# Kernel tuning notes

Hardware: AMD Instinct MI355X
Metric: run time of the kernel (lower is better)

Reference implementation:

```python
import jax, jax.numpy as jnp
import numpy as np

NEG_SLOPE = 0.2  # PyG GATConv default leaky_relu slope
EPS = 1e-16


def gat_conv(x, W, att_src, att_dst, bias, src, dst, heads, out_ch, concat):
    """PyG-style GATConv (eval mode, self-loops already added).
    x: [N, F_in], W: [F_in, heads*out_ch], att_src/att_dst: [heads, out_ch], bias matches output.
    src/dst: [E] int edge endpoints (messages flow src -> dst).
    """
    N = x.shape[0]
    h = (x @ W).reshape(N, heads, out_ch)                 # [N, H, C]
    a_src = jnp.einsum('nhc,hc->nh', h, att_src)           # [N, H]
    a_dst = jnp.einsum('nhc,hc->nh', h, att_dst)           # [N, H]
    e = jax.nn.leaky_relu(a_src[src] + a_dst[dst], NEG_SLOPE)  # [E, H]
    # scatter-softmax over edges grouped by destination node
    emax = jax.ops.segment_max(e, dst, num_segments=N)     # [N, H]
    e = jnp.exp(e - emax[dst])
    denom = jax.ops.segment_sum(e, dst, num_segments=N)    # [N, H]
    alpha = e / (denom[dst] + EPS)                         # [E, H]
    msg = alpha[:, :, None] * h[src]                       # [E, H, C]
    out = jax.ops.segment_sum(msg, dst, num_segments=N)    # [N, H, C]
    out = out.reshape(N, heads * out_ch) if concat else out.mean(axis=1)
    return out + bias


def _add_self_loops(edge_index, N):
    loop = jnp.arange(N, dtype=edge_index.dtype)
    src = jnp.concatenate([edge_index[0], loop])
    dst = jnp.concatenate([edge_index[1], loop])
    return src, dst


def setup_inputs() -> dict:
    key = jax.random.key(0)
    ks = jax.random.split(key, 12)
    N, F_in, E = 100000, 256, 3200000
    H1, C1 = 2, 16
    C2 = 40  # num_classes
    x = jax.random.normal(ks[0], (N, F_in), dtype=jnp.float32)
    edge_index = jax.random.randint(ks[1], (2, E), 0, N, dtype=jnp.int32)
    s1 = 1.0 / np.sqrt(F_in)
    s2 = 1.0 / np.sqrt(H1 * C1)
    W1 = jax.random.normal(ks[2], (F_in, H1 * C1), dtype=jnp.float32) * s1
    att_src1 = jax.random.normal(ks[3], (H1, C1), dtype=jnp.float32) * s2
    att_dst1 = jax.random.normal(ks[4], (H1, C1), dtype=jnp.float32) * s2
    b1 = jnp.zeros((H1 * C1,), dtype=jnp.float32)
    W2 = jax.random.normal(ks[5], (H1 * C1, C2), dtype=jnp.float32) * s2
    att_src2 = jax.random.normal(ks[6], (1, C2), dtype=jnp.float32) * 0.15
    att_dst2 = jax.random.normal(ks[7], (1, C2), dtype=jnp.float32) * 0.15
    b2 = jnp.zeros((C2,), dtype=jnp.float32)
    return {"x": x, "edge_index": edge_index, "W1": W1, "att_src1": att_src1,
            "att_dst1": att_dst1, "b1": b1, "W2": W2, "att_src2": att_src2,
            "att_dst2": att_dst2, "b2": b2}


def reference(x, edge_index, W1, att_src1, att_dst1, b1, W2, att_src2, att_dst2, b2):
    N = x.shape[0]
    src, dst = _add_self_loops(edge_index, N)
    h = gat_conv(x, W1, att_src1, att_dst1, b1, src, dst, heads=2, out_ch=16, concat=True)
    h = jax.nn.relu(h)
    # F.dropout / attention dropout are identity in eval mode
    out = gat_conv(h, W2, att_src2, att_dst2, b2, src, dst, heads=1, out_ch=40, concat=False)
    return jax.nn.log_softmax(out, axis=1)
```

## Files before the change

### kernel.cpp

```cpp
#include <hip/hip_runtime.h>
#include <math.h>

#define FIN 256
#define F1  32
#define H1  2
#define C1  16
#define C2  40
#define MAXDEG 96
#define NEG_SLOPE 0.2f
#define GAT_EPS 1e-16f
#define G1_NODES 32
#define FILL_BLOCKS 2048

__device__ __forceinline__ float lrelu(float v) { return v >= 0.f ? v : NEG_SLOPE * v; }

__global__ __launch_bounds__(256) void k_fill_adj(const int* __restrict__ ei, int E, int N,
                                                  int* __restrict__ deg, int* __restrict__ adj) {
    int res = blockIdx.x & 7;
    int nper = (N + 7) >> 3;
    int lo = res * nper;
    int hi = min(N, lo + nper);
    int total = E + N;
    int stride = (gridDim.x >> 3) * blockDim.x;
    for (int j = (blockIdx.x >> 3) * blockDim.x + threadIdx.x; j < total; j += stride) {
        int d, s;
        if (j < E) {
            d = __builtin_nontemporal_load(&ei[E + j]);
            s = 0;
            if (d >= lo && d < hi) s = __builtin_nontemporal_load(&ei[j]);
        } else {
            d = j - E; s = d;
        }
        if (d >= lo && d < hi) {
            int pos = atomicAdd(&deg[d], 1);
            if (pos < MAXDEG) adj[d * MAXDEG + pos] = s;
        }
    }
}

__global__ __launch_bounds__(256) void k_gemm1(const float* __restrict__ x,
                                               const float* __restrict__ W1,
                                               const float* __restrict__ attS,
                                               const float* __restrict__ attD,
                                               float* __restrict__ h1,
                                               float* __restrict__ aS,
                                               float* __restrict__ aD, int N) {
    __shared__ float xs[G1_NODES * FIN];
    __shared__ float Ws[FIN * F1];
    int tid = threadIdx.x;
    int node0 = blockIdx.x * G1_NODES;

    const float4* W4 = (const float4*)W1;
    float4* Ws4 = (float4*)Ws;
    for (int i = tid; i < FIN * F1 / 4; i += 256) Ws4[i] = W4[i];

    const float4* x4 = (const float4*)x;
    float4* xs4 = (float4*)xs;
    for (int i = tid; i < G1_NODES * FIN / 4; i += 256) {
        int r = i >> 6;
        int n = node0 + r;
        float4 v = make_float4(0.f, 0.f, 0.f, 0.f);
        if (n < N) v = x4[(size_t)n * 64 + (i & 63)];
        xs4[i] = v;
    }
    __syncthreads();

    int ln = tid >> 3;
    int c0 = (tid & 7) * 4;
    float a0 = 0.f, a1 = 0.f, a2 = 0.f, a3 = 0.f;
    for (int k = 0; k < FIN; k += 4) {
        float4 xv = *(const float4*)&xs[ln * FIN + k];
        float4 w0 = *(const float4*)&Ws[(k + 0) * F1 + c0];
        float4 w1 = *(const float4*)&Ws[(k + 1) * F1 + c0];
        float4 w2 = *(const float4*)&Ws[(k + 2) * F1 + c0];
        float4 w3 = *(const float4*)&Ws[(k + 3) * F1 + c0];
        a0 += xv.x * w0.x + xv.y * w1.x + xv.z * w2.x + xv.w * w3.x;
        a1 += xv.x * w0.y + xv.y * w1.y + xv.z * w2.y + xv.w * w3.y;
        a2 += xv.x * w0.z + xv.y * w1.z + xv.z * w2.z + xv.w * w3.z;
        a3 += xv.x * w0.w + xv.y * w1.w + xv.z * w2.w + xv.w * w3.w;
    }

    float4 sv = *(const float4*)&attS[c0];
    float4 dv = *(const float4*)&attD[c0];
    float ps = a0 * sv.x + a1 * sv.y + a2 * sv.z + a3 * sv.w;
    float pd = a0 * dv.x + a1 * dv.y + a2 * dv.z + a3 * dv.w;
    ps += __shfl_xor(ps, 1); ps += __shfl_xor(ps, 2);
    pd += __shfl_xor(pd, 1); pd += __shfl_xor(pd, 2);
    float po = __shfl_xor(ps, 4);
    float qo = __shfl_xor(pd, 4);

    int n = node0 + ln;
    if (n < N) {
        *(float4*)&h1[(size_t)n * F1 + c0] = make_float4(a0, a1, a2, a3);
        if ((tid & 7) == 0) {
            *(float2*)&aS[2 * (size_t)n] = make_float2(ps, po);
            *(float2*)&aD[2 * (size_t)n] = make_float2(pd, qo);
        }
    }
}

__global__ __launch_bounds__(256) void k_agg1(const float* __restrict__ h1,
                                              const int* __restrict__ adj,
                                              const int* __restrict__ deg,
                                              const float* __restrict__ aS,
                                              const float* __restrict__ aD,
                                              const float* __restrict__ b1,
                                              float* __restrict__ h1r, int N) {
    int warp = threadIdx.x >> 6;
    int lane = threadIdx.x & 63;
    int node = blockIdx.x * 4 + warp;
    if (node >= N) return;
    int dg = min(deg[node], MAXDEG);
    float2 adp = *(const float2*)&aD[node * 2];
    const int* ap = adj + (size_t)node * MAXDEG;

    int s0 = 0, s1 = 0;
    float e00 = -INFINITY, e01 = -INFINITY, e10 = -INFINITY, e11 = -INFINITY;
    if (lane < dg) {
        s0 = ap[lane];
        float2 as = *(const float2*)&aS[2 * s0];
        e00 = lrelu(as.x + adp.x); e01 = lrelu(as.y + adp.y);
    }
    if (lane + 64 < dg) {
        s1 = ap[lane + 64];
        float2 as = *(const float2*)&aS[2 * s1];
        e10 = lrelu(as.x + adp.x); e11 = lrelu(as.y + adp.y);
    }
    float m0 = fmaxf(e00, e10), m1 = fmaxf(e01, e11);
#pragma unroll
    for (int off = 32; off; off >>= 1) {
        m0 = fmaxf(m0, __shfl_xor(m0, off));
        m1 = fmaxf(m1, __shfl_xor(m1, off));
    }
    float w00 = (lane < dg)      ? __expf(e00 - m0) : 0.f;
    float w01 = (lane < dg)      ? __expf(e01 - m1) : 0.f;
    float w10 = (lane + 64 < dg) ? __expf(e10 - m0) : 0.f;
    float w11 = (lane + 64 < dg) ? __expf(e11 - m1) : 0.f;
    float sw0 = w00 + w10, sw1 = w01 + w11;
#pragma unroll
    for (int off = 32; off; off >>= 1) {
        sw0 += __shfl_xor(sw0, off);
        sw1 += __shfl_xor(sw1, off);
    }

    int eg = lane >> 3;
    int cg = lane & 7;
    int head = cg >> 2;
    float4 acc = make_float4(0.f, 0.f, 0.f, 0.f);
    for (int j0 = 0; j0 < dg; j0 += 8) {
        int j = j0 + eg;
        int sl = j & 63;
        int s; float w;
        if (j0 < 64) {
            s = __shfl(s0, sl);
            float wA = __shfl(w00, sl);
            float wB = __shfl(w01, sl);
            w = head ? wB : wA;
        } else {
            s = __shfl(s1, sl);
            float wA = __shfl(w10, sl);
            float wB = __shfl(w11, sl);
            w = head ? wB : wA;
        }
        float4 hv = *(const float4*)&h1[(size_t)s * F1 + cg * 4];
        acc.x += w * hv.x; acc.y += w * hv.y; acc.z += w * hv.z; acc.w += w * hv.w;
    }
#pragma unroll
    for (int off = 8; off < 64; off <<= 1) {
        acc.x += __shfl_xor(acc.x, off);
        acc.y += __shfl_xor(acc.y, off);
        acc.z += __shfl_xor(acc.z, off);
        acc.w += __shfl_xor(acc.w, off);
    }
    if (eg == 0) {
        float swh = head ? sw1 : sw0;
        float inv = 1.f / (swh + GAT_EPS);
        float4 bv = *(const float4*)&b1[cg * 4];
        float4 o;
        o.x = fmaxf(acc.x * inv + bv.x, 0.f);
        o.y = fmaxf(acc.y * inv + bv.y, 0.f);
        o.z = fmaxf(acc.z * inv + bv.z, 0.f);
        o.w = fmaxf(acc.w * inv + bv.w, 0.f);
        *(float4*)&h1r[(size_t)node * F1 + cg * 4] = o;
    }
}

__global__ __launch_bounds__(320) void k_gemm2(const float* __restrict__ h1r,
                                               const float* __restrict__ W2,
                                               float* __restrict__ h2, int N) {
    __shared__ float hs[8 * F1];
    __shared__ float Ws[F1 * C2];
    int tid = threadIdx.x;
    int node0 = blockIdx.x * 8;
    for (int i = tid; i < F1 * C2; i += 320) Ws[i] = W2[i];
    if (tid < 8 * F1) {
        int r = tid >> 5;
        int n = node0 + r;
        hs[tid] = (n < N) ? h1r[(size_t)n * F1 + (tid & 31)] : 0.f;
    }
    __syncthreads();
    int node = tid / C2;
    int col  = tid - node * C2;
    int n = node0 + node;
    if (n < N) {
        float acc = 0.f;
#pragma unroll
        for (int k = 0; k < F1; k++) acc += hs[node * F1 + k] * Ws[k * C2 + col];
        h2[(size_t)n * C2 + col] = acc;
    }
}

__global__ void k_attdots2(const float* __restrict__ h2,
                           const float* __restrict__ attS, const float* __restrict__ attD,
                           float* __restrict__ aS, float* __restrict__ aD, int N) {
    int n = blockIdx.x * blockDim.x + threadIdx.x;
    if (n >= N) return;
    const float* hp = h2 + (size_t)n * C2;
    float s = 0.f, d = 0.f;
#pragma unroll
    for (int c = 0; c < C2; c++) { float v = hp[c]; s += v * attS[c]; d += v * attD[c]; }
    aS[n] = s; aD[n] = d;
}

__global__ __launch_bounds__(256) void k_agg2(const float* __restrict__ h2,
                                              const int* __restrict__ adj,
                                              const int* __restrict__ deg,
                                              const float* __restrict__ aS,
                                              const float* __restrict__ aD,
                                              const float* __restrict__ b2,
                                              float* __restrict__ out, int N) {
    int warp = threadIdx.x >> 6;
    int lane = threadIdx.x & 63;
    int node = blockIdx.x * 4 + warp;
    if (node >= N) return;
    int dg = min(deg[node], MAXDEG);
    float ad = aD[node];
    const int* ap = adj + (size_t)node * MAXDEG;

    int s0 = 0, s1 = 0;
    float e0 = -INFINITY, e1 = -INFINITY;
    if (lane < dg)      { s0 = ap[lane];      e0 = lrelu(aS[s0] + ad); }
    if (lane + 64 < dg) { s1 = ap[lane + 64]; e1 = lrelu(aS[s1] + ad); }
    float m = fmaxf(e0, e1);
#pragma unroll
    for (int off = 32; off; off >>= 1) m = fmaxf(m, __shfl_xor(m, off));
    float w0 = (lane < dg)      ? __expf(e0 - m) : 0.f;
    float w1 = (lane + 64 < dg) ? __expf(e1 - m) : 0.f;
    float sw = w0 + w1;
#pragma unroll
    for (int off = 32; off; off >>= 1) sw += __shfl_xor(sw, off);

    int eg = lane >> 3;
    int cg = lane & 7;
    float4 acc = make_float4(0.f, 0.f, 0.f, 0.f);
    float acc4 = 0.f;
    for (int j0 = 0; j0 < dg; j0 += 8) {
        int j = j0 + eg;
        int sl = j & 63;
        int s; float w;
        if (j0 < 64) { s = __shfl(s0, sl); w = __shfl(w0, sl); }
        else         { s = __shfl(s1, sl); w = __shfl(w1, sl); }
        const float* hp = &h2[(size_t)s * C2];
        float4 hv = *(const float4*)&hp[cg * 4];
        float  h5 = hp[32 + cg];
        acc.x += w * hv.x; acc.y += w * hv.y; acc.z += w * hv.z; acc.w += w * hv.w;
        acc4  += w * h5;
    }
#pragma unroll
    for (int off = 8; off < 64; off <<= 1) {
        acc.x += __shfl_xor(acc.x, off);
        acc.y += __shfl_xor(acc.y, off);
        acc.z += __shfl_xor(acc.z, off);
        acc.w += __shfl_xor(acc.w, off);
        acc4  += __shfl_xor(acc4, off);
    }
    float inv = 1.f / (sw + GAT_EPS);
    float4 bv = *(const float4*)&b2[cg * 4];
    float  b5 = b2[32 + cg];
    float v0 = acc.x * inv + bv.x;
    float v1 = acc.y * inv + bv.y;
    float v2 = acc.z * inv + bv.z;
    float v3 = acc.w * inv + bv.w;
    float v4 = acc4  * inv + b5;

    float lm = fmaxf(fmaxf(fmaxf(v0, v1), fmaxf(v2, v3)), v4);
#pragma unroll
    for (int off = 1; off < 8; off <<= 1) lm = fmaxf(lm, __shfl_xor(lm, off));
    float ex = __expf(v0 - lm) + __expf(v1 - lm) + __expf(v2 - lm) +
               __expf(v3 - lm) + __expf(v4 - lm);
#pragma unroll
    for (int off = 1; off < 8; off <<= 1) ex += __shfl_xor(ex, off);
    float lse = lm + __logf(ex);
    if (eg == 0) {
        float* op = out + (size_t)node * C2;
        float4 o = make_float4(v0 - lse, v1 - lse, v2 - lse, v3 - lse);
        *(float4*)&op[cg * 4] = o;
        op[32 + cg] = v4 - lse;
    }
}

extern "C" void kernel_launch(void* const* d_in, const int* in_sizes, int n_in,
                              void* d_out, int out_size, void* d_ws, size_t ws_size,
                              hipStream_t stream) {
    const float* x    = (const float*)d_in[0];
    const int*   ei   = (const int*)d_in[1];
    const float* W1   = (const float*)d_in[2];
    const float* aS1w = (const float*)d_in[3];
    const float* aD1w = (const float*)d_in[4];
    const float* b1   = (const float*)d_in[5];
    const float* W2   = (const float*)d_in[6];
    const float* aS2w = (const float*)d_in[7];
    const float* aD2w = (const float*)d_in[8];
    const float* b2   = (const float*)d_in[9];
    const int N = in_sizes[0] / FIN;
    const int E = in_sizes[1] / 2;

    char* ws = (char*)d_ws;
    size_t off = 0;
    auto alloc = [&](size_t bytes) -> void* {
        void* p = ws + off;
        off = (off + bytes + 511) & ~(size_t)511;
        return p;
    };
    int*   deg = (int*)alloc(sizeof(int) * (size_t)N);
    int*   adj = (int*)alloc(sizeof(int) * (size_t)N * MAXDEG);
    float* h1  = (float*)alloc(sizeof(float) * (size_t)N * F1);
    float* aS1 = (float*)alloc(sizeof(float) * (size_t)N * H1);
    float* aD1 = (float*)alloc(sizeof(float) * (size_t)N * H1);
    float* h1r = (float*)alloc(sizeof(float) * (size_t)N * F1);
    float* h2  = (float*)alloc(sizeof(float) * (size_t)N * C2);
    float* aS2 = (float*)alloc(sizeof(float) * (size_t)N);
    float* aD2 = (float*)alloc(sizeof(float) * (size_t)N);

    hipMemsetAsync(deg, 0, sizeof(int) * (size_t)N, stream);
    k_fill_adj<<<FILL_BLOCKS, 256, 0, stream>>>(ei, E, N, deg, adj);
    k_gemm1<<<(N + G1_NODES - 1) / G1_NODES, 256, 0, stream>>>(x, W1, aS1w, aD1w, h1, aS1, aD1, N);
    k_agg1<<<(N + 3) / 4, 256, 0, stream>>>(h1, adj, deg, aS1, aD1, b1, h1r, N);
    k_gemm2<<<(N + 7) / 8, 320, 0, stream>>>(h1r, W2, h2, N);
    k_attdots2<<<(N + 255) / 256, 256, 0, stream>>>(h2, aS2w, aD2w, aS2, aD2, N);
    k_agg2<<<(N + 3) / 4, 256, 0, stream>>>(h2, adj, deg, aS2, aD2, b2, (float*)d_out, N);
}
```

Measured before the change: 574.5 us.

## Merge adjacency fill with gemm1 and fuse layer-2 attention dots into gemm2

The adjacency-fill and first GEMM now run in one launch, with block ranges split between the two roles so the memory-bound atomic scatter can overlap the x@W1 compute. The gemm1 path drops its LDS staging and reads x and W1 straight from global memory through the cache. The separate attdots2 kernel is removed; gemm2 instead reduces the per-node att_src/att_dst dot products with LDS atomics and writes them directly, saving a pass over h2. The risks are that gemm1 without shared memory may become bound on global loads, and that the LDS float atomics add contention.

```diff
diff --git a/kernel.cpp b/kernel.cpp
--- a/kernel.cpp
+++ b/kernel.cpp
@@ -14,66 +14,56 @@
 
 __device__ __forceinline__ float lrelu(float v) { return v >= 0.f ? v : NEG_SLOPE * v; }
 
-__global__ __launch_bounds__(256) void k_fill_adj(const int* __restrict__ ei, int E, int N,
-                                                  int* __restrict__ deg, int* __restrict__ adj) {
-    int res = blockIdx.x & 7;
-    int nper = (N + 7) >> 3;
-    int lo = res * nper;
-    int hi = min(N, lo + nper);
-    int total = E + N;
-    int stride = (gridDim.x >> 3) * blockDim.x;
-    for (int j = (blockIdx.x >> 3) * blockDim.x + threadIdx.x; j < total; j += stride) {
-        int d, s;
-        if (j < E) {
-            d = __builtin_nontemporal_load(&ei[E + j]);
-            s = 0;
-            if (d >= lo && d < hi) s = __builtin_nontemporal_load(&ei[j]);
-        } else {
-            d = j - E; s = d;
-        }
-        if (d >= lo && d < hi) {
+__global__ __launch_bounds__(256) void k_fill_gemm1(const int* __restrict__ ei, int E,
+                                                    const float* __restrict__ x,
+                                                    const float* __restrict__ W1,
+                                                    const float* __restrict__ attS,
+                                                    const float* __restrict__ attD,
+                                                    int* __restrict__ deg,
+                                                    int* __restrict__ adj,
+                                                    float* __restrict__ h1,
+                                                    float* __restrict__ aS,
+                                                    float* __restrict__ aD, int N) {
+    if (blockIdx.x < FILL_BLOCKS) {
+        int res = blockIdx.x & 7;
+        int nper = (N + 7) >> 3;
+        int lo = res * nper;
+        int hi = min(N, lo + nper);
+        int total = E + N;
+        int stride = (FILL_BLOCKS >> 3) * 256;
+        for (int j = (blockIdx.x >> 3) * 256 + threadIdx.x; j < total; j += stride) {
+            int d, s;
+            if (j < E) {
+                d = __builtin_nontemporal_load(&ei[E + j]);
+                if (d < lo || d >= hi) continue;
+                s = __builtin_nontemporal_load(&ei[j]);
+            } else {
+                d = j - E; s = d;
+                if (d < lo || d >= hi) continue;
+            }
             int pos = atomicAdd(&deg[d], 1);
             if (pos < MAXDEG) adj[d * MAXDEG + pos] = s;
         }
-    }
-}
-
-__global__ __launch_bounds__(256) void k_gemm1(const float* __restrict__ x,
-                                               const float* __restrict__ W1,
-                                               const float* __restrict__ attS,
-                                               const float* __restrict__ attD,
-                                               float* __restrict__ h1,
-                                               float* __restrict__ aS,
-                                               float* __restrict__ aD, int N) {
-    __shared__ float xs[G1_NODES * FIN];
-    __shared__ float Ws[FIN * F1];
+        return;
+    }
+
     int tid = threadIdx.x;
-    int node0 = blockIdx.x * G1_NODES;
-
-    const float4* W4 = (const float4*)W1;
-    float4* Ws4 = (float4*)Ws;
-    for (int i = tid; i < FIN * F1 / 4; i += 256) Ws4[i] = W4[i];
-
-    const float4* x4 = (const float4*)x;
-    float4* xs4 = (float4*)xs;
-    for (int i = tid; i < G1_NODES * FIN / 4; i += 256) {
-        int r = i >> 6;
-        int n = node0 + r;
-        float4 v = make_float4(0.f, 0.f, 0.f, 0.f);
-        if (n < N) v = x4[(size_t)n * 64 + (i & 63)];
-        xs4[i] = v;
-    }
-    __syncthreads();
-
+    int node0 = (blockIdx.x - FILL_BLOCKS) * G1_NODES;
     int ln = tid >> 3;
     int c0 = (tid & 7) * 4;
+    int n = node0 + ln;
+    bool valid = n < N;
+
+    const float4* xr = (const float4*)(x + (size_t)n * FIN);
+    const float4* Wr = (const float4*)W1;
     float a0 = 0.f, a1 = 0.f, a2 = 0.f, a3 = 0.f;
+#pragma unroll 4
     for (int k = 0; k < FIN; k += 4) {
-        float4 xv = *(const float4*)&xs[ln * FIN + k];
-        float4 w0 = *(const float4*)&Ws[(k + 0) * F1 + c0];
-        float4 w1 = *(const float4*)&Ws[(k + 1) * F1 + c0];
-        float4 w2 = *(const float4*)&Ws[(k + 2) * F1 + c0];
-        float4 w3 = *(const float4*)&Ws[(k + 3) * F1 + c0];
+        float4 xv = valid ? xr[k >> 2] : make_float4(0.f, 0.f, 0.f, 0.f);
+        float4 w0 = Wr[(k + 0) * 8 + (c0 >> 2)];
+        float4 w1 = Wr[(k + 1) * 8 + (c0 >> 2)];
+        float4 w2 = Wr[(k + 2) * 8 + (c0 >> 2)];
+        float4 w3 = Wr[(k + 3) * 8 + (c0 >> 2)];
         a0 += xv.x * w0.x + xv.y * w1.x + xv.z * w2.x + xv.w * w3.x;
         a1 += xv.x * w0.y + xv.y * w1.y + xv.z * w2.y + xv.w * w3.y;
         a2 += xv.x * w0.z + xv.y * w1.z + xv.z * w2.z + xv.w * w3.z;
@@ -89,8 +79,7 @@
     float po = __shfl_xor(ps, 4);
     float qo = __shfl_xor(pd, 4);
 
-    int n = node0 + ln;
-    if (n < N) {
+    if (valid) {
         *(float4*)&h1[(size_t)n * F1 + c0] = make_float4(a0, a1, a2, a3);
         if ((tid & 7) == 0) {
             *(float2*)&aS[2 * (size_t)n] = make_float2(ps, po);
@@ -187,9 +176,14 @@
 
 __global__ __launch_bounds__(320) void k_gemm2(const float* __restrict__ h1r,
                                                const float* __restrict__ W2,
-                                               float* __restrict__ h2, int N) {
+                                               const float* __restrict__ attS,
+                                               const float* __restrict__ attD,
+                                               float* __restrict__ h2,
+                                               float* __restrict__ aS,
+                                               float* __restrict__ aD, int N) {
     __shared__ float hs[8 * F1];
     __shared__ float Ws[F1 * C2];
+    __shared__ float ldsS[8], ldsD[8];
     int tid = threadIdx.x;
     int node0 = blockIdx.x * 8;
     for (int i = tid; i < F1 * C2; i += 320) Ws[i] = W2[i];
@@ -198,28 +192,22 @@
         int n = node0 + r;
         hs[tid] = (n < N) ? h1r[(size_t)n * F1 + (tid & 31)] : 0.f;
     }
+    if (tid < 8) { ldsS[tid] = 0.f; ldsD[tid] = 0.f; }
     __syncthreads();
     int node = tid / C2;
     int col  = tid - node * C2;
     int n = node0 + node;
-    if (n < N) {
-        float acc = 0.f;
-#pragma unroll
-        for (int k = 0; k < F1; k++) acc += hs[node * F1 + k] * Ws[k * C2 + col];
-        h2[(size_t)n * C2 + col] = acc;
-    }
-}
-
-__global__ void k_attdots2(const float* __restrict__ h2,
-                           const float* __restrict__ attS, const float* __restrict__ attD,
-                           float* __restrict__ aS, float* __restrict__ aD, int N) {
-    int n = blockIdx.x * blockDim.x + threadIdx.x;
-    if (n >= N) return;
-    const float* hp = h2 + (size_t)n * C2;
-    float s = 0.f, d = 0.f;
-#pragma unroll
-    for (int c = 0; c < C2; c++) { float v = hp[c]; s += v * attS[c]; d += v * attD[c]; }
-    aS[n] = s; aD[n] = d;
+    float acc = 0.f;
+#pragma unroll
+    for (int k = 0; k < F1; k++) acc += hs[node * F1 + k] * Ws[k * C2 + col];
+    if (n < N) h2[(size_t)n * C2 + col] = acc;
+    atomicAdd(&ldsS[node], acc * attS[col]);
+    atomicAdd(&ldsD[node], acc * attD[col]);
+    __syncthreads();
+    if (tid < 8 && node0 + tid < N) {
+        aS[node0 + tid] = ldsS[tid];
+        aD[node0 + tid] = ldsD[tid];
+    }
 }
 
 __global__ __launch_bounds__(256) void k_agg2(const float* __restrict__ h2,
@@ -333,10 +321,10 @@
     float* aD2 = (float*)alloc(sizeof(float) * (size_t)N);
 
     hipMemsetAsync(deg, 0, sizeof(int) * (size_t)N, stream);
-    k_fill_adj<<<FILL_BLOCKS, 256, 0, stream>>>(ei, E, N, deg, adj);
-    k_gemm1<<<(N + G1_NODES - 1) / G1_NODES, 256, 0, stream>>>(x, W1, aS1w, aD1w, h1, aS1, aD1, N);
+    int gemm_blocks = (N + G1_NODES - 1) / G1_NODES;
+    k_fill_gemm1<<<FILL_BLOCKS + gemm_blocks, 256, 0, stream>>>(
+        ei, E, x, W1, aS1w, aD1w, deg, adj, h1, aS1, aD1, N);
     k_agg1<<<(N + 3) / 4, 256, 0, stream>>>(h1, adj, deg, aS1, aD1, b1, h1r, N);
-    k_gemm2<<<(N + 7) / 8, 320, 0, stream>>>(h1r, W2, h2, N);
-    k_attdots2<<<(N + 255) / 256, 256, 0, stream>>>(h2, aS2w, aD2w, aS2, aD2, N);
+    k_gemm2<<<(N + 7) / 8, 320, 0, stream>>>(h1r, W2, aS2w, aD2w, h2, aS2, aD2, N);
     k_agg2<<<(N + 3) / 4, 256, 0, stream>>>(h2, adj, deg, aS2, aD2, b2, (float*)d_out, N);
 }
```

Measured after the change: 722.4 us. 1.26x slower.
